# Performance work log

Measured on AMD Instinct MI355X. Metric: run time of the kernel, lower is better.

The kernel has to match this reference:

```python
import jax, jax.numpy as jnp
import numpy as np

MARGIN = 0.5        # contrastive margin (init kwarg)
NUM_LABELS = 20     # label ids are in [0, NUM_LABELS)


def setup_inputs() -> dict:
    key = jax.random.key(0)
    k1, k2 = jax.random.split(key)
    emb = jax.random.normal(k1, (4, 16, 64, 64), dtype=jnp.float32)
    lab = jax.random.randint(k2, (4, 64, 64), 0, NUM_LABELS, dtype=jnp.int32)
    return {"emb": emb, "lab": lab}


def _loss_one(x, y):
    # x: (C, H, W) embedding, y: (H, W) int labels
    C, H, W = x.shape
    N = H * W
    xf = x.reshape(C, N)
    # per-pixel centering across channels, then L2-normalize across channels
    xc = xf - jnp.mean(xf, axis=0, keepdims=True)
    nrm = jnp.sqrt(jnp.sum(xc * xc, axis=0))           # (N,)
    denom = jnp.where(nrm > 0, nrm, 1.0)
    e = jnp.where(nrm > 0, xc / denom, 0.0).T          # (N, C); NaN-mask -> 0
    sim = (e @ e.T) * 0.5 + 0.5                        # (N, N) in [0, 1]

    yi = y.reshape(N)
    yf = yi.astype(jnp.float32) + 1.0
    eq = yf[:, None] == yf[None, :]
    nz = (yf[:, None] * yf[None, :]) != 0.0            # product-zero exclusion (faithful)
    lp = jnp.where(nz, jnp.where(eq, 1.0, -1.0), 0.0)  # label-pair matrix

    # inverse-frequency per-pixel weights, outer product for pairs
    cnt = jnp.zeros((NUM_LABELS,), jnp.float32).at[yi].add(1.0)
    wpix = 1.0 / cnt[yi]                               # (N,)
    Wm = wpix[:, None] * wpix[None, :]                 # (N, N)

    # positive pairs: relu(1 - sim); negative pairs: relu(sim - margin)
    loss = jnp.where(lp == 1.0, jnp.maximum(1.0 - sim, 0.0),
                     jnp.where(lp == -1.0, jnp.maximum(sim - MARGIN, 0.0), 0.0))
    return jnp.sum(Wm * loss) / N


def reference(emb, lab):
    return jnp.sum(jax.vmap(_loss_one)(emb, lab))
```

## Files before the change

### kernel.cpp

```cpp
#include <hip/hip_runtime.h>

#define NUM_LABELS 20
#define N_PIX 4096
#define C_DIM 16
#define BATCH 4

#define PTILE 128
#define PNT (N_PIX / PTILE)
#define PTPAIRS (PNT * (PNT + 1) / 2)
#define NPAIRS (BATCH * PTPAIRS)

#define PREP_SLICES 16
#define NPREP (BATCH * PREP_SLICES)
#define NPART (NPREP + NPAIRS)

typedef __attribute__((ext_vector_type(8))) short bf16x8;
typedef __attribute__((ext_vector_type(4))) float f32x4;

__device__ __forceinline__ unsigned int bf16rne(float f) {
    unsigned int x = __float_as_uint(f);
    return (x + 0x7fffu + ((x >> 16) & 1u)) >> 16;
}

__global__ __launch_bounds__(256) void prep_kernel(
    const float* __restrict__ emb,
    const int*   __restrict__ lab,
    unsigned short* __restrict__ gT,
    float* __restrict__ part)
{
    const int blk  = blockIdx.x;
    const int b    = blk / PREP_SLICES;
    const int sl   = blk % PREP_SLICES;
    const int t    = threadIdx.x;
    const int wv   = t >> 6;
    const int lane = t & 63;

    __shared__ int   h[NUM_LABELS];
    __shared__ float rinv[NUM_LABELS];
    __shared__ float wsum[4];

    if (t < NUM_LABELS) h[t] = 0;
    __syncthreads();

    {
        const int* yb = lab + (size_t)b * N_PIX;
        int cnt[NUM_LABELS];
#pragma unroll
        for (int l = 0; l < NUM_LABELS; ++l) cnt[l] = 0;
        for (int it = 0; it < 16; ++it) {
            const int y = yb[wv * 1024 + it * 64 + lane];
#pragma unroll
            for (int l = 0; l < NUM_LABELS; ++l)
                cnt[l] += (int)__popcll(__ballot(y == l));
        }
        if (lane == 0) {
#pragma unroll
            for (int l = 0; l < NUM_LABELS; ++l) atomicAdd(&h[l], cnt[l]);
        }
    }
    __syncthreads();
    if (t < NUM_LABELS) rinv[t] = (h[t] > 0) ? 1.0f / (float)h[t] : 0.0f;
    __syncthreads();

    const int n = sl * 256 + t;
    const float* xb = emb + (size_t)b * C_DIM * N_PIX + n;
    float v[C_DIM];
    float s = 0.f;
#pragma unroll
    for (int c = 0; c < C_DIM; ++c) { v[c] = xb[(size_t)c * N_PIX]; s += v[c]; }
    const float mean = s * (1.0f / C_DIM);
    float ss = 0.f;
#pragma unroll
    for (int c = 0; c < C_DIM; ++c) { v[c] -= mean; ss += v[c] * v[c]; }
    const float nrm = sqrtf(ss);
    const float w   = rinv[lab[(size_t)b * N_PIX + n]];
    const float inv = (nrm > 0.f) ? (w / nrm) : 0.f;

    unsigned int u[8];
#pragma unroll
    for (int k = 0; k < 8; ++k) {
        const unsigned int lo = bf16rne(v[2 * k] * inv);
        const unsigned int hi = bf16rne(v[2 * k + 1] * inv);
        u[k] = lo | (hi << 16);
    }
    unsigned int* gp = (unsigned int*)(gT + ((size_t)b * N_PIX + n) * C_DIM);
    *reinterpret_cast<uint4*>(gp)     = make_uint4(u[0], u[1], u[2], u[3]);
    *reinterpret_cast<uint4*>(gp + 4) = make_uint4(u[4], u[5], u[6], u[7]);

    float sq = inv * inv * ss;
#pragma unroll
    for (int off = 32; off > 0; off >>= 1) sq += __shfl_down(sq, off);
    if (lane == 0) wsum[wv] = sq;
    __syncthreads();
    if (t == 0) {
        float e = -0.5f * (wsum[0] + wsum[1] + wsum[2] + wsum[3]);
        if (sl == 0) {
            int p = 0;
#pragma unroll
            for (int l = 0; l < NUM_LABELS; ++l) p += (h[l] > 0) ? 1 : 0;
            e += 0.5f * (float)p;
        }
        part[blk] = e;
    }
}

__global__ __launch_bounds__(256) void pair_kernel(
    const unsigned short* __restrict__ gT,
    const int*   __restrict__ lab,
    float* __restrict__ part)
{
    const int p  = blockIdx.x;
    const int b  = p / PTPAIRS;
    const int k0 = p % PTPAIRS;

    const float nn = (float)PNT;
    int ti = (int)(((2.f * nn + 1.f) -
                    sqrtf((2.f * nn + 1.f) * (2.f * nn + 1.f) - 8.f * (float)k0)) * 0.5f);
    if (ti < 0) ti = 0;
    if (ti > PNT - 1) ti = PNT - 1;
    auto rowoff = [](int r) { return r * PNT - (r * (r - 1)) / 2; };
    while (ti > 0 && k0 < rowoff(ti)) --ti;
    while (ti < PNT - 1 && k0 >= rowoff(ti + 1)) ++ti;
    const int tj = ti + (k0 - rowoff(ti));
    const bool diag = (ti == tj);

    const int t    = threadIdx.x;
    const int wv   = t >> 6;
    const int lane = t & 63;
    const int lo16 = lane & 15;
    const int hi   = lane >> 4;
    const bool doread = (hi < 2);

    const unsigned short* gb = gT + (size_t)b * N_PIX * C_DIM;
    const int* lb = lab + (size_t)b * N_PIX;

    bf16x8 afrag[2] = {bf16x8{}, bf16x8{}};
    int    yIr[2][4];
#pragma unroll
    for (int rt = 0; rt < 2; ++rt) {
        const int rtile = wv * 2 + rt;
        const int arow  = ti * PTILE + rtile * 16 + lo16;
        if (doread)
            afrag[rt] = *reinterpret_cast<const bf16x8*>(gb + (size_t)arow * C_DIM + hi * 8);
        const int4 yv = *reinterpret_cast<const int4*>(lb + ti * PTILE + rtile * 16 + hi * 4);
        yIr[rt][0] = yv.x; yIr[rt][1] = yv.y; yIr[rt][2] = yv.z; yIr[rt][3] = yv.w;
    }

    float sum = 0.f;
#pragma unroll
    for (int ct = 0; ct < 8; ++ct) {
        const int brow = tj * PTILE + ct * 16 + lo16;
        bf16x8 bfrag = bf16x8{};
        if (doread)
            bfrag = *reinterpret_cast<const bf16x8*>(gb + (size_t)brow * C_DIM + hi * 8);
        const int yq = lb[tj * PTILE + ct * 16 + lo16];
#pragma unroll
        for (int rt = 0; rt < 2; ++rt) {
            const int rtile = wv * 2 + rt;
            if (diag && rtile > ct) continue;
            f32x4 acc = {0.f, 0.f, 0.f, 0.f};
            acc = __builtin_amdgcn_mfma_f32_16x16x32_bf16(afrag[rt], bfrag, acc, 0, 0, 0);
            if (diag && rtile == ct) {
#pragma unroll
                for (int j = 0; j < 4; ++j) {
                    const float s = acc[j];
                    const float v = (yIr[rt][j] == yq) ? -s : fmaxf(s, 0.f);
                    const int iloc = hi * 4 + j;
                    sum += (iloc < lo16) ? v : 0.f;
                }
            } else {
#pragma unroll
                for (int j = 0; j < 4; ++j) {
                    const float s = acc[j];
                    sum += (yIr[rt][j] == yq) ? -s : fmaxf(s, 0.f);
                }
            }
        }
    }

#pragma unroll
    for (int off = 32; off > 0; off >>= 1) sum += __shfl_down(sum, off);
    __shared__ float wred[4];
    if (lane == 0) wred[wv] = sum;
    __syncthreads();
    if (t == 0) part[NPREP + p] = wred[0] + wred[1] + wred[2] + wred[3];
}

__global__ __launch_bounds__(256) void reduce_kernel(
    const float* __restrict__ part, float* __restrict__ out)
{
    __shared__ double sd[256];
    const int t = threadIdx.x;
    double s = 0.0;
    for (int i = t; i < NPART; i += 256) s += (double)part[i];
    sd[t] = s;
    __syncthreads();
#pragma unroll
    for (int k = 128; k > 0; k >>= 1) {
        if (t < k) sd[t] += sd[t + k];
        __syncthreads();
    }
    if (t == 0) out[0] = (float)(sd[0] * (1.0 / (double)N_PIX));
}

extern "C" void kernel_launch(void* const* d_in, const int* in_sizes, int n_in,
                              void* d_out, int out_size, void* d_ws, size_t ws_size,
                              hipStream_t stream) {
    const float* emb = (const float*)d_in[0];
    const int*   lab = (const int*)d_in[1];
    float* out = (float*)d_out;

    unsigned short* gT = (unsigned short*)d_ws;
    float* part = (float*)(gT + (size_t)BATCH * N_PIX * C_DIM);

    prep_kernel<<<NPREP, 256, 0, stream>>>(emb, lab, gT, part);
    pair_kernel<<<NPAIRS, 256, 0, stream>>>(gT, lab, part);
    reduce_kernel<<<1, 256, 0, stream>>>(part, out);
}
```

Before: 26.04 us.

## Fuse final reduction into pair kernel via atomics and loop batches per block

Drops the separate reduce kernel: prep zeroes the output and each pair block atomically adds its scaled partial, with block 0 also folding in the prep partials. Pair blocks now cover one tile pair across all four batches, with 512 threads staging both tiles into padded shared memory, one 16-row tile per wave. This removes a launch and spreads global loads across threads, at the cost of fewer blocks, a serial batch loop with barriers, and float atomics whose summation order is nondeterministic.

```diff
diff --git a/kernel.cpp b/kernel.cpp
--- a/kernel.cpp
+++ b/kernel.cpp
@@ -8,11 +8,9 @@
 #define PTILE 128
 #define PNT (N_PIX / PTILE)
 #define PTPAIRS (PNT * (PNT + 1) / 2)
-#define NPAIRS (BATCH * PTPAIRS)
-
 #define PREP_SLICES 16
 #define NPREP (BATCH * PREP_SLICES)
-#define NPART (NPREP + NPAIRS)
+#define KPAD 24
 
 typedef __attribute__((ext_vector_type(8))) short bf16x8;
 typedef __attribute__((ext_vector_type(4))) float f32x4;
@@ -26,7 +24,8 @@
     const float* __restrict__ emb,
     const int*   __restrict__ lab,
     unsigned short* __restrict__ gT,
-    float* __restrict__ part)
+    float* __restrict__ part,
+    float* __restrict__ out)
 {
     const int blk  = blockIdx.x;
     const int b    = blk / PREP_SLICES;
@@ -35,6 +34,8 @@
     const int wv   = t >> 6;
     const int lane = t & 63;
 
+    if (blk == 0 && t == 0) out[0] = 0.f;
+
     __shared__ int   h[NUM_LABELS];
     __shared__ float rinv[NUM_LABELS];
     __shared__ float wsum[4];
@@ -104,14 +105,13 @@
     }
 }
 
-__global__ __launch_bounds__(256) void pair_kernel(
+__global__ __launch_bounds__(512) void pair_kernel(
     const unsigned short* __restrict__ gT,
     const int*   __restrict__ lab,
-    float* __restrict__ part)
+    const float* __restrict__ part,
+    float* __restrict__ out)
 {
-    const int p  = blockIdx.x;
-    const int b  = p / PTPAIRS;
-    const int k0 = p % PTPAIRS;
+    const int k0 = blockIdx.x;
 
     const float nn = (float)PNT;
     int ti = (int)(((2.f * nn + 1.f) -
@@ -131,40 +131,65 @@
     const int hi   = lane >> 4;
     const bool doread = (hi < 2);
 
-    const unsigned short* gb = gT + (size_t)b * N_PIX * C_DIM;
-    const int* lb = lab + (size_t)b * N_PIX;
-
-    bf16x8 afrag[2] = {bf16x8{}, bf16x8{}};
-    int    yIr[2][4];
-#pragma unroll
-    for (int rt = 0; rt < 2; ++rt) {
-        const int rtile = wv * 2 + rt;
-        const int arow  = ti * PTILE + rtile * 16 + lo16;
+    __shared__ unsigned short sI[PTILE * KPAD];
+    __shared__ unsigned short sJ[PTILE * KPAD];
+    __shared__ int   syI[PTILE], syJ[PTILE];
+    __shared__ float wred[8];
+
+    float sum = 0.f;
+
+    if (k0 == 0 && t < NPREP) {
+        float e = part[t];
+#pragma unroll
+        for (int off = 32; off > 0; off >>= 1) e += __shfl_down(e, off);
+        if (t == 0) sum += e;
+    }
+
+    for (int b = 0; b < BATCH; ++b) {
+        __syncthreads();
+
+        const unsigned short* gb = gT + (size_t)b * N_PIX * C_DIM;
+        {
+            const int u2  = t & 255;
+            const int row = u2 >> 1, half = u2 & 1;
+            const int tile = (t < 256) ? ti : tj;
+            unsigned short* dst = (t < 256) ? sI : sJ;
+            const uint4 vv = *(reinterpret_cast<const uint4*>(
+                gb + (size_t)(tile * PTILE + row) * C_DIM) + half);
+            *reinterpret_cast<uint4*>(&dst[row * KPAD + half * 8]) = vv;
+        }
+        if (t < PTILE) {
+            syI[t] = lab[(size_t)b * N_PIX + ti * PTILE + t];
+        } else if (t < 2 * PTILE) {
+            const int u = t - PTILE;
+            syJ[u] = lab[(size_t)b * N_PIX + tj * PTILE + u];
+        }
+        __syncthreads();
+
+        const int rtile = wv;
+        bf16x8 afrag = bf16x8{};
         if (doread)
-            afrag[rt] = *reinterpret_cast<const bf16x8*>(gb + (size_t)arow * C_DIM + hi * 8);
-        const int4 yv = *reinterpret_cast<const int4*>(lb + ti * PTILE + rtile * 16 + hi * 4);
-        yIr[rt][0] = yv.x; yIr[rt][1] = yv.y; yIr[rt][2] = yv.z; yIr[rt][3] = yv.w;
-    }
-
-    float sum = 0.f;
-#pragma unroll
-    for (int ct = 0; ct < 8; ++ct) {
-        const int brow = tj * PTILE + ct * 16 + lo16;
-        bf16x8 bfrag = bf16x8{};
-        if (doread)
-            bfrag = *reinterpret_cast<const bf16x8*>(gb + (size_t)brow * C_DIM + hi * 8);
-        const int yq = lb[tj * PTILE + ct * 16 + lo16];
-#pragma unroll
-        for (int rt = 0; rt < 2; ++rt) {
-            const int rtile = wv * 2 + rt;
+            afrag = *reinterpret_cast<const bf16x8*>(&sI[(rtile * 16 + lo16) * KPAD + hi * 8]);
+        int yIr[4];
+        {
+            const int4 yv = *reinterpret_cast<const int4*>(&syI[rtile * 16 + hi * 4]);
+            yIr[0] = yv.x; yIr[1] = yv.y; yIr[2] = yv.z; yIr[3] = yv.w;
+        }
+
+#pragma unroll
+        for (int ct = 0; ct < 8; ++ct) {
             if (diag && rtile > ct) continue;
+            bf16x8 bfrag = bf16x8{};
+            if (doread)
+                bfrag = *reinterpret_cast<const bf16x8*>(&sJ[(ct * 16 + lo16) * KPAD + hi * 8]);
+            const int yq = syJ[ct * 16 + lo16];
             f32x4 acc = {0.f, 0.f, 0.f, 0.f};
-            acc = __builtin_amdgcn_mfma_f32_16x16x32_bf16(afrag[rt], bfrag, acc, 0, 0, 0);
+            acc = __builtin_amdgcn_mfma_f32_16x16x32_bf16(afrag, bfrag, acc, 0, 0, 0);
             if (diag && rtile == ct) {
 #pragma unroll
                 for (int j = 0; j < 4; ++j) {
                     const float s = acc[j];
-                    const float v = (yIr[rt][j] == yq) ? -s : fmaxf(s, 0.f);
+                    const float v = (yIr[j] == yq) ? -s : fmaxf(s, 0.f);
                     const int iloc = hi * 4 + j;
                     sum += (iloc < lo16) ? v : 0.f;
                 }
@@ -172,7 +197,7 @@
 #pragma unroll
                 for (int j = 0; j < 4; ++j) {
                     const float s = acc[j];
-                    sum += (yIr[rt][j] == yq) ? -s : fmaxf(s, 0.f);
+                    sum += (yIr[j] == yq) ? -s : fmaxf(s, 0.f);
                 }
             }
         }
@@ -180,27 +205,14 @@
 
 #pragma unroll
     for (int off = 32; off > 0; off >>= 1) sum += __shfl_down(sum, off);
-    __shared__ float wred[4];
     if (lane == 0) wred[wv] = sum;
     __syncthreads();
-    if (t == 0) part[NPREP + p] = wred[0] + wred[1] + wred[2] + wred[3];
-}
-
-__global__ __launch_bounds__(256) void reduce_kernel(
-    const float* __restrict__ part, float* __restrict__ out)
-{
-    __shared__ double sd[256];
-    const int t = threadIdx.x;
-    double s = 0.0;
-    for (int i = t; i < NPART; i += 256) s += (double)part[i];
-    sd[t] = s;
-    __syncthreads();
-#pragma unroll
-    for (int k = 128; k > 0; k >>= 1) {
-        if (t < k) sd[t] += sd[t + k];
-        __syncthreads();
-    }
-    if (t == 0) out[0] = (float)(sd[0] * (1.0 / (double)N_PIX));
+    if (t == 0) {
+        float total = 0.f;
+#pragma unroll
+        for (int i = 0; i < 8; ++i) total += wred[i];
+        atomicAdd(out, total * (1.0f / (float)N_PIX));
+    }
 }
 
 extern "C" void kernel_launch(void* const* d_in, const int* in_sizes, int n_in,
@@ -213,7 +225,6 @@
     unsigned short* gT = (unsigned short*)d_ws;
     float* part = (float*)(gT + (size_t)BATCH * N_PIX * C_DIM);
 
-    prep_kernel<<<NPREP, 256, 0, stream>>>(emb, lab, gT, part);
-    pair_kernel<<<NPAIRS, 256, 0, stream>>>(gT, lab, part);
-    reduce_kernel<<<1, 256, 0, stream>>>(part, out);
-}
+    prep_kernel<<<NPREP, 256, 0, stream>>>(emb, lab, gT, part, out);
+    pair_kernel<<<PTPAIRS, 512, 0, stream>>>(gT, lab, part, out);
+}
```

After: 28.89 us. 10.9% more time.
